# Performance work log

Hardware: AMD Instinct MI355X
Metric: run time of the kernel (lower is better)

Reference implementation:

```python
import jax, jax.numpy as jnp
import numpy as np

N, C, D = 32768, 2048, 512

def setup_inputs() -> dict:
    key = jax.random.key(0)
    k1, k2, k3 = jax.random.split(key, 3)
    X = jax.random.normal(k1, (N, D), dtype=jnp.float32)
    muK = jax.random.normal(k2, (C, D), dtype=jnp.float32)
    # counts per class; zeros mark 'unvisited' classes exercising the masking path
    cK = jax.random.randint(k3, (C,), 0, 3).astype(jnp.float32)
    return {"X": X, "muK": muK, "cK": cK}

def reference(X, muK, cK):
    # find_dists(A=muK, B=X): dist[i, j] = sum_d (muK[j, d] - X[i, d])**2, scores = -dist
    # avoids materializing the N x C x D broadcast intermediate of the original).
    x2 = jnp.sum(X * X, axis=1, keepdims=True)          # (N, 1)
    m2 = jnp.sum(muK * muK, axis=1)                     # (C,)
    scores = -(x2 + m2[None, :] - 2.0 * (X @ muK.T))    # (N, C)
    # unvisited classes (cK == 0) get per-row min score minus 1
    min_col = jnp.min(scores, axis=1, keepdims=True) - 1.0  # (N, 1)
    scores = jnp.where((cK == 0.0)[None, :], min_col, scores)
    # predict(..., return_probas=True) as used in evaluate_
    return jax.nn.softmax(scores, axis=1)
```

## Files before the change

kernel.cpp:

```cpp
#include <hip/hip_runtime.h>
#include <cfloat>

#define N_ROWS 32768
#define N_CLS  2048
#define DIM    512

#define LDR 40

typedef __attribute__((ext_vector_type(8))) short short8;
typedef __attribute__((ext_vector_type(4))) short short4v;
typedef __attribute__((ext_vector_type(4))) float f32x4;

__device__ __forceinline__ unsigned f2bf_bits(float x) {
    union { float f; unsigned u; } a; a.f = x;
    return (a.u + 0x7fffu + ((a.u >> 16) & 1u)) >> 16;
}
__device__ __forceinline__ float bf_to_f(unsigned bits) {
    union { unsigned u; float f; } a; a.u = bits << 16;
    return a.f;
}
__device__ __forceinline__ void split_bf(float x, short &h, short &l) {
    unsigned hb = f2bf_bits(x);
    h = (short)hb;
    float r = x - bf_to_f(hb);
    l = (short)f2bf_bits(r);
}

__global__ __launch_bounds__(256) void m2_kernel(const float* __restrict__ muK,
                                                 float* __restrict__ m2) {
    const int j = blockIdx.x;
    const int t = threadIdx.x;
    const float* r = muK + (size_t)j * DIM;
    float a = r[t], b = r[t + 256];
    float s = a * a + b * b;
    for (int off = 32; off; off >>= 1) s += __shfl_xor(s, off);
    __shared__ float sw[4];
    if ((t & 63) == 0) sw[t >> 6] = s;
    __syncthreads();
    if (t == 0) m2[j] = sw[0] + sw[1] + sw[2] + sw[3];
}

__global__ __launch_bounds__(256) void gemm_kernel(const float* __restrict__ X,
                                                   const float* __restrict__ muK,
                                                   const float* __restrict__ m2,
                                                   float* __restrict__ S) {
    __shared__ __align__(16) short Ah[128 * LDR];
    __shared__ __align__(16) short Al[128 * LDR];
    __shared__ __align__(16) short Bh[128 * LDR];
    __shared__ __align__(16) short Bl[128 * LDR];

    const int tid  = threadIdx.x;
    const int n0   = blockIdx.x * 128;
    const int m0   = blockIdx.y * 128;
    const int w    = tid >> 6;
    const int lane = tid & 63;
    const int wm   = (w >> 1) * 64;
    const int wn   = (w & 1) * 64;
    const int l16  = lane & 15;
    const int quad = lane >> 4;

    f32x4 acc[4][4];
#pragma unroll
    for (int mt = 0; mt < 4; ++mt)
#pragma unroll
        for (int nt = 0; nt < 4; ++nt)
            acc[mt][nt] = (f32x4){0.f, 0.f, 0.f, 0.f};

    for (int kt = 0; kt < DIM; kt += 32) {
        __syncthreads();
#pragma unroll
        for (int i = 0; i < 4; ++i) {
            int idx = tid + 256 * i;
            int row = idx >> 3;
            int c4  = (idx & 7) * 4;
            float4 fa = *(const float4*)(X + (size_t)(m0 + row) * DIM + kt + c4);
            float4 fb = *(const float4*)(muK + (size_t)(n0 + row) * DIM + kt + c4);
            short h0, h1, h2, h3, l0, l1, l2, l3;
            split_bf(fa.x, h0, l0); split_bf(fa.y, h1, l1);
            split_bf(fa.z, h2, l2); split_bf(fa.w, h3, l3);
            *(short4v*)&Ah[row * LDR + c4] = (short4v){h0, h1, h2, h3};
            *(short4v*)&Al[row * LDR + c4] = (short4v){l0, l1, l2, l3};
            split_bf(fb.x, h0, l0); split_bf(fb.y, h1, l1);
            split_bf(fb.z, h2, l2); split_bf(fb.w, h3, l3);
            *(short4v*)&Bh[row * LDR + c4] = (short4v){h0, h1, h2, h3};
            *(short4v*)&Bl[row * LDR + c4] = (short4v){l0, l1, l2, l3};
        }
        __syncthreads();
        short8 ah[4], al[4];
#pragma unroll
        for (int mt = 0; mt < 4; ++mt) {
            int r = wm + mt * 16 + l16;
            ah[mt] = *(const short8*)&Ah[r * LDR + quad * 8];
            al[mt] = *(const short8*)&Al[r * LDR + quad * 8];
        }
#pragma unroll
        for (int nt = 0; nt < 4; ++nt) {
            int r = wn + nt * 16 + l16;
            short8 bh = *(const short8*)&Bh[r * LDR + quad * 8];
            short8 bl = *(const short8*)&Bl[r * LDR + quad * 8];
#pragma unroll
            for (int mt = 0; mt < 4; ++mt)
                acc[mt][nt] = __builtin_amdgcn_mfma_f32_16x16x32_bf16(ah[mt], bh, acc[mt][nt], 0, 0, 0);
#pragma unroll
            for (int mt = 0; mt < 4; ++mt)
                acc[mt][nt] = __builtin_amdgcn_mfma_f32_16x16x32_bf16(ah[mt], bl, acc[mt][nt], 0, 0, 0);
#pragma unroll
            for (int mt = 0; mt < 4; ++mt)
                acc[mt][nt] = __builtin_amdgcn_mfma_f32_16x16x32_bf16(al[mt], bh, acc[mt][nt], 0, 0, 0);
        }
    }

#pragma unroll
    for (int nt = 0; nt < 4; ++nt) {
        int col = n0 + wn + nt * 16 + l16;
        float mm = m2[col];
#pragma unroll
        for (int mt = 0; mt < 4; ++mt) {
            int rbase = m0 + wm + mt * 16 + quad * 4;
#pragma unroll
            for (int r = 0; r < 4; ++r)
                S[(size_t)(rbase + r) * N_CLS + col] = 2.0f * acc[mt][nt][r] - mm;
        }
    }
}

__global__ __launch_bounds__(256) void softmax_kernel(float* __restrict__ S,
                                                      const float* __restrict__ cK) {
    const int row = blockIdx.x;
    float* p = S + (size_t)row * N_CLS;
    const int t = threadIdx.x;

    float v[8];
    bool  msk[8];
    float mn = FLT_MAX, mx = -FLT_MAX;
#pragma unroll
    for (int i = 0; i < 8; ++i) {
        int c = t + 256 * i;
        float s = p[c];
        v[i] = s;
        bool m = (cK[c] == 0.0f);
        msk[i] = m;
        mn = fminf(mn, s);
        if (!m) mx = fmaxf(mx, s);
    }
    for (int off = 32; off; off >>= 1) {
        mn = fminf(mn, __shfl_xor(mn, off));
        mx = fmaxf(mx, __shfl_xor(mx, off));
    }
    __shared__ float smn[4], smx[4], ssum[4];
    const int wid = t >> 6;
    if ((t & 63) == 0) { smn[wid] = mn; smx[wid] = mx; }
    __syncthreads();
    mn = fminf(fminf(smn[0], smn[1]), fminf(smn[2], smn[3]));
    mx = fmaxf(fmaxf(smx[0], smx[1]), fmaxf(smx[2], smx[3]));
    if (mx == -FLT_MAX) mx = mn - 1.0f;
    const float fill = mn - 1.0f;

    float e[8];
    float sum = 0.f;
#pragma unroll
    for (int i = 0; i < 8; ++i) {
        float val = msk[i] ? fill : v[i];
        e[i] = __expf(val - mx);
        sum += e[i];
    }
    for (int off = 32; off; off >>= 1) sum += __shfl_xor(sum, off);
    if ((t & 63) == 0) ssum[wid] = sum;
    __syncthreads();
    sum = ssum[0] + ssum[1] + ssum[2] + ssum[3];
    const float inv = 1.0f / sum;
#pragma unroll
    for (int i = 0; i < 8; ++i)
        p[t + 256 * i] = e[i] * inv;
}

extern "C" void kernel_launch(void* const* d_in, const int* in_sizes, int n_in,
                              void* d_out, int out_size, void* d_ws, size_t ws_size,
                              hipStream_t stream) {
    const float* X   = (const float*)d_in[0];
    const float* muK = (const float*)d_in[1];
    const float* cK  = (const float*)d_in[2];
    float* out = (float*)d_out;
    float* m2  = (float*)d_ws;

    m2_kernel<<<N_CLS, 256, 0, stream>>>(muK, m2);
    dim3 grid(N_CLS / 128, N_ROWS / 128);
    gemm_kernel<<<grid, 256, 0, stream>>>(X, muK, m2, out);
    softmax_kernel<<<N_ROWS, 256, 0, stream>>>(out, cK);
}
```

Measured before the change: 654.6 us.

## Pre-split inputs to bf16 hi/lo and stream them into LDS with global_load_lds

Adds a pre-pass that splits X and muK once into bf16 high and low arrays in workspace. The GEMM then loads tiles directly into LDS with global_load_lds over three passes (hi*hi, hi*lo, lo*hi), so the per-tile conversion and the register staging disappear. The softmax now uses one wavefront per row with float4 loads, which drops the shared-memory reductions and block barriers. In exchange it needs extra workspace, adds extra memory traffic for the split arrays, and uses an unpadded LDS layout that may cause bank conflicts; a fallback path keeps the old GEMM when workspace is too small.

```diff
diff --git a/kernel.cpp b/kernel.cpp
--- a/kernel.cpp
+++ b/kernel.cpp
@@ -4,8 +4,6 @@
 #define N_ROWS 32768
 #define N_CLS  2048
 #define DIM    512
-
-#define LDR 40
 
 typedef __attribute__((ext_vector_type(8))) short short8;
 typedef __attribute__((ext_vector_type(4))) short short4v;
@@ -24,6 +22,18 @@
     h = (short)hb;
     float r = x - bf_to_f(hb);
     l = (short)f2bf_bits(r);
+}
+
+__global__ __launch_bounds__(256) void split_kernel(const float* __restrict__ src,
+                                                    short* __restrict__ hi,
+                                                    short* __restrict__ lo) {
+    int idx = blockIdx.x * 256 + threadIdx.x;
+    float4 v = ((const float4*)src)[idx];
+    short h0, h1, h2, h3, l0, l1, l2, l3;
+    split_bf(v.x, h0, l0); split_bf(v.y, h1, l1);
+    split_bf(v.z, h2, l2); split_bf(v.w, h3, l3);
+    ((short4v*)hi)[idx] = (short4v){h0, h1, h2, h3};
+    ((short4v*)lo)[idx] = (short4v){l0, l1, l2, l3};
 }
 
 __global__ __launch_bounds__(256) void m2_kernel(const float* __restrict__ muK,
@@ -40,14 +50,18 @@
     if (t == 0) m2[j] = sw[0] + sw[1] + sw[2] + sw[3];
 }
 
-__global__ __launch_bounds__(256) void gemm_kernel(const float* __restrict__ X,
-                                                   const float* __restrict__ muK,
+#define GLDS16(g, l) __builtin_amdgcn_global_load_lds( \
+    (const __attribute__((address_space(1))) unsigned int*)(g), \
+    (__attribute__((address_space(3))) unsigned int*)(l), 16, 0, 0)
+
+__global__ __launch_bounds__(256) void gemm_kernel(const short* __restrict__ Xh,
+                                                   const short* __restrict__ Xl,
+                                                   const short* __restrict__ Mh,
+                                                   const short* __restrict__ Ml,
                                                    const float* __restrict__ m2,
                                                    float* __restrict__ S) {
-    __shared__ __align__(16) short Ah[128 * LDR];
-    __shared__ __align__(16) short Al[128 * LDR];
-    __shared__ __align__(16) short Bh[128 * LDR];
-    __shared__ __align__(16) short Bl[128 * LDR];
+    __shared__ __align__(16) short As[128 * 32];
+    __shared__ __align__(16) short Bs[128 * 32];
 
     const int tid  = threadIdx.x;
     const int n0   = blockIdx.x * 128;
@@ -59,6 +73,13 @@
     const int l16  = lane & 15;
     const int quad = lane >> 4;
 
+    const int c0 = w * 128 + lane;
+    const int c1 = c0 + 64;
+    const size_t ga0 = (size_t)(m0 + (c0 >> 2)) * DIM + (c0 & 3) * 8;
+    const size_t ga1 = (size_t)(m0 + (c1 >> 2)) * DIM + (c1 & 3) * 8;
+    const size_t gb0 = (size_t)(n0 + (c0 >> 2)) * DIM + (c0 & 3) * 8;
+    const size_t gb1 = (size_t)(n0 + (c1 >> 2)) * DIM + (c1 & 3) * 8;
+
     f32x4 acc[4][4];
 #pragma unroll
     for (int mt = 0; mt < 4; ++mt)
@@ -66,6 +87,72 @@
         for (int nt = 0; nt < 4; ++nt)
             acc[mt][nt] = (f32x4){0.f, 0.f, 0.f, 0.f};
 
+#pragma unroll 1
+    for (int seg = 0; seg < 3; ++seg) {
+        const short* Ap = (seg == 2) ? Xl : Xh;
+        const short* Bp = (seg == 1) ? Ml : Mh;
+#pragma unroll 1
+        for (int kt2 = 0; kt2 < 16; ++kt2) {
+            const int kk = kt2 * 32;
+            __syncthreads();
+            GLDS16(Ap + ga0 + kk, &As[c0 * 8]);
+            GLDS16(Ap + ga1 + kk, &As[c1 * 8]);
+            GLDS16(Bp + gb0 + kk, &Bs[c0 * 8]);
+            GLDS16(Bp + gb1 + kk, &Bs[c1 * 8]);
+            __syncthreads();
+
+            short8 ah[4];
+#pragma unroll
+            for (int mt = 0; mt < 4; ++mt)
+                ah[mt] = *(const short8*)&As[(wm + mt * 16 + l16) * 32 + quad * 8];
+#pragma unroll
+            for (int nt = 0; nt < 4; ++nt) {
+                short8 bf = *(const short8*)&Bs[(wn + nt * 16 + l16) * 32 + quad * 8];
+#pragma unroll
+                for (int mt = 0; mt < 4; ++mt)
+                    acc[mt][nt] = __builtin_amdgcn_mfma_f32_16x16x32_bf16(ah[mt], bf, acc[mt][nt], 0, 0, 0);
+            }
+        }
+    }
+
+#pragma unroll
+    for (int nt = 0; nt < 4; ++nt) {
+        int col = n0 + wn + nt * 16 + l16;
+        float mm = m2[col];
+#pragma unroll
+        for (int mt = 0; mt < 4; ++mt) {
+            int rbase = m0 + wm + mt * 16 + quad * 4;
+#pragma unroll
+            for (int r = 0; r < 4; ++r)
+                S[(size_t)(rbase + r) * N_CLS + col] = 2.0f * acc[mt][nt][r] - mm;
+        }
+    }
+}
+
+#define LDR 40
+__global__ __launch_bounds__(256) void gemm_fallback(const float* __restrict__ X,
+                                                     const float* __restrict__ muK,
+                                                     const float* __restrict__ m2,
+                                                     float* __restrict__ S) {
+    __shared__ __align__(16) short Ah[128 * LDR];
+    __shared__ __align__(16) short Al[128 * LDR];
+    __shared__ __align__(16) short Bh[128 * LDR];
+    __shared__ __align__(16) short Bl[128 * LDR];
+    const int tid  = threadIdx.x;
+    const int n0   = blockIdx.x * 128;
+    const int m0   = blockIdx.y * 128;
+    const int w    = tid >> 6;
+    const int lane = tid & 63;
+    const int wm   = (w >> 1) * 64;
+    const int wn   = (w & 1) * 64;
+    const int l16  = lane & 15;
+    const int quad = lane >> 4;
+    f32x4 acc[4][4];
+#pragma unroll
+    for (int mt = 0; mt < 4; ++mt)
+#pragma unroll
+        for (int nt = 0; nt < 4; ++nt)
+            acc[mt][nt] = (f32x4){0.f, 0.f, 0.f, 0.f};
     for (int kt = 0; kt < DIM; kt += 32) {
         __syncthreads();
 #pragma unroll
@@ -109,7 +196,6 @@
                 acc[mt][nt] = __builtin_amdgcn_mfma_f32_16x16x32_bf16(al[mt], bh, acc[mt][nt], 0, 0, 0);
         }
     }
-
 #pragma unroll
     for (int nt = 0; nt < 4; ++nt) {
         int col = n0 + wn + nt * 16 + l16;
@@ -126,52 +212,52 @@
 
 __global__ __launch_bounds__(256) void softmax_kernel(float* __restrict__ S,
                                                       const float* __restrict__ cK) {
-    const int row = blockIdx.x;
-    float* p = S + (size_t)row * N_CLS;
-    const int t = threadIdx.x;
-
-    float v[8];
-    bool  msk[8];
+    const int row  = blockIdx.x * 4 + (threadIdx.x >> 6);
+    const int lane = threadIdx.x & 63;
+    float4* p = (float4*)(S + (size_t)row * N_CLS);
+    const float4* ck4 = (const float4*)cK;
+
+    float4 v[8];
+    unsigned msk = 0;
     float mn = FLT_MAX, mx = -FLT_MAX;
 #pragma unroll
     for (int i = 0; i < 8; ++i) {
-        int c = t + 256 * i;
-        float s = p[c];
+        int c = i * 64 + lane;
+        float4 s = p[c];
+        float4 k = ck4[c];
         v[i] = s;
-        bool m = (cK[c] == 0.0f);
-        msk[i] = m;
-        mn = fminf(mn, s);
-        if (!m) mx = fmaxf(mx, s);
+        if (k.x == 0.f) msk |= 1u << (i * 4 + 0); else mx = fmaxf(mx, s.x);
+        if (k.y == 0.f) msk |= 1u << (i * 4 + 1); else mx = fmaxf(mx, s.y);
+        if (k.z == 0.f) msk |= 1u << (i * 4 + 2); else mx = fmaxf(mx, s.z);
+        if (k.w == 0.f) msk |= 1u << (i * 4 + 3); else mx = fmaxf(mx, s.w);
+        mn = fminf(mn, fminf(fminf(s.x, s.y), fminf(s.z, s.w)));
     }
     for (int off = 32; off; off >>= 1) {
         mn = fminf(mn, __shfl_xor(mn, off));
         mx = fmaxf(mx, __shfl_xor(mx, off));
     }
-    __shared__ float smn[4], smx[4], ssum[4];
-    const int wid = t >> 6;
-    if ((t & 63) == 0) { smn[wid] = mn; smx[wid] = mx; }
-    __syncthreads();
-    mn = fminf(fminf(smn[0], smn[1]), fminf(smn[2], smn[3]));
-    mx = fmaxf(fmaxf(smx[0], smx[1]), fmaxf(smx[2], smx[3]));
     if (mx == -FLT_MAX) mx = mn - 1.0f;
     const float fill = mn - 1.0f;
 
-    float e[8];
     float sum = 0.f;
 #pragma unroll
     for (int i = 0; i < 8; ++i) {
-        float val = msk[i] ? fill : v[i];
-        e[i] = __expf(val - mx);
-        sum += e[i];
+        float4 s = v[i];
+        s.x = __expf(((msk >> (i * 4 + 0)) & 1u ? fill : s.x) - mx);
+        s.y = __expf(((msk >> (i * 4 + 1)) & 1u ? fill : s.y) - mx);
+        s.z = __expf(((msk >> (i * 4 + 2)) & 1u ? fill : s.z) - mx);
+        s.w = __expf(((msk >> (i * 4 + 3)) & 1u ? fill : s.w) - mx);
+        sum += s.x + s.y + s.z + s.w;
+        v[i] = s;
     }
     for (int off = 32; off; off >>= 1) sum += __shfl_xor(sum, off);
-    if ((t & 63) == 0) ssum[wid] = sum;
-    __syncthreads();
-    sum = ssum[0] + ssum[1] + ssum[2] + ssum[3];
     const float inv = 1.0f / sum;
 #pragma unroll
-    for (int i = 0; i < 8; ++i)
-        p[t + 256 * i] = e[i] * inv;
+    for (int i = 0; i < 8; ++i) {
+        float4 s = v[i];
+        s.x *= inv; s.y *= inv; s.z *= inv; s.w *= inv;
+        p[i * 64 + lane] = s;
+    }
 }
 
 extern "C" void kernel_launch(void* const* d_in, const int* in_sizes, int n_in,
@@ -181,10 +267,27 @@
     const float* muK = (const float*)d_in[1];
     const float* cK  = (const float*)d_in[2];
     float* out = (float*)d_out;
-    float* m2  = (float*)d_ws;
-
-    m2_kernel<<<N_CLS, 256, 0, stream>>>(muK, m2);
-    dim3 grid(N_CLS / 128, N_ROWS / 128);
-    gemm_kernel<<<grid, 256, 0, stream>>>(X, muK, m2, out);
-    softmax_kernel<<<N_ROWS, 256, 0, stream>>>(out, cK);
-}
+
+    const size_t XN = (size_t)N_ROWS * DIM;
+    const size_t MN = (size_t)N_CLS * DIM;
+    short* Xh = (short*)d_ws;
+    short* Xl = Xh + XN;
+    short* Mh = Xl + XN;
+    short* Ml = Mh + MN;
+    float* m2 = (float*)(Ml + MN);
+    const size_t need = (2 * XN + 2 * MN) * sizeof(short) + N_CLS * sizeof(float);
+
+    if (ws_size >= need) {
+        split_kernel<<<(int)(XN / 4 / 256), 256, 0, stream>>>(X, Xh, Xl);
+        split_kernel<<<(int)(MN / 4 / 256), 256, 0, stream>>>(muK, Mh, Ml);
+        m2_kernel<<<N_CLS, 256, 0, stream>>>(muK, m2);
+        dim3 grid(N_CLS / 128, N_ROWS / 128);
+        gemm_kernel<<<grid, 256, 0, stream>>>(Xh, Xl, Mh, Ml, m2, out);
+    } else {
+        float* m2f = (float*)d_ws;
+        m2_kernel<<<N_CLS, 256, 0, stream>>>(muK, m2f);
+        dim3 grid(N_CLS / 128, N_ROWS / 128);
+        gemm_fallback<<<grid, 256, 0, stream>>>(X, muK, m2f, out);
+    }
+    softmax_kernel<<<N_ROWS / 4, 256, 0, stream>>>(out, cK);
+}
```

Result: faster. 641.7 us (-2.0%).
